# Kernel tuning notes

Hardware: AMD Instinct MI355X
Metric: run time of the kernel (lower is better)

Reference implementation:

```python
import jax, jax.numpy as jnp
import numpy as np
import math

D_MODEL = 1024
N_HEADS = 16
D_K = D_MODEL // N_HEADS
ROPE_BASE = 10000.0


def rope_cos_sin(seq_len, d_k, base=ROPE_BASE, dtype=jnp.float32):
    inv_freq = 1.0 / base ** (jnp.arange(0, d_k, 2, dtype=dtype) / d_k)  # [d_k/2]
    pos = jnp.arange(seq_len, dtype=dtype)
    freqs = jnp.outer(pos, inv_freq)  # [T, d_k/2]
    return jnp.cos(freqs), jnp.sin(freqs)


def apply_rope(x, cos, sin):
    # x: [B, H, T, d_k]; cos/sin: [T, d_k/2]
    x1 = x[..., 0::2]
    x2 = x[..., 1::2]
    c = cos[None, None]
    s = sin[None, None]
    r1 = x1 * c - x2 * s
    r2 = x1 * s + x2 * c
    return jnp.stack([r1, r2], axis=-1).reshape(x.shape)


def setup_inputs() -> dict:
    key = jax.random.key(0)
    ks = jax.random.split(key, 7)
    B, T = 2, 2048
    scale = 1.0 / math.sqrt(D_MODEL)
    return {
        "query": jax.random.normal(ks[0], (B, T, D_MODEL), jnp.float32),
        "key": jax.random.normal(ks[1], (B, T, D_MODEL), jnp.float32),
        "value": jax.random.normal(ks[2], (B, T, D_MODEL), jnp.float32),
        "Wq": jax.random.normal(ks[3], (D_MODEL, D_MODEL), jnp.float32) * scale,
        "Wk": jax.random.normal(ks[4], (D_MODEL, D_MODEL), jnp.float32) * scale,
        "Wv": jax.random.normal(ks[5], (D_MODEL, D_MODEL), jnp.float32) * scale,
        "Wo": jax.random.normal(ks[6], (D_MODEL, D_MODEL), jnp.float32) * scale,
    }


def reference(query, key, value, Wq, Wk, Wv, Wo):
    B, Tq, _ = query.shape
    Tk = key.shape[1]
    # nn.Linear: x @ W.T
    Q = (query @ Wq.T).reshape(B, Tq, N_HEADS, D_K).transpose(0, 2, 1, 3)
    K = (key @ Wk.T).reshape(B, Tk, N_HEADS, D_K).transpose(0, 2, 1, 3)
    V = (value @ Wv.T).reshape(B, Tk, N_HEADS, D_K).transpose(0, 2, 1, 3)
    cos_q, sin_q = rope_cos_sin(Tq, D_K)
    cos_k, sin_k = rope_cos_sin(Tk, D_K)
    Q = apply_rope(Q, cos_q, sin_q)
    K = apply_rope(K, cos_k, sin_k)
    scores = jnp.einsum("bhqd,bhkd->bhqk", Q, K) / math.sqrt(D_K)
    attn = jax.nn.softmax(scores, axis=-1)
    out = jnp.einsum("bhqk,bhkd->bhqd", attn, V)
    out = out.transpose(0, 2, 1, 3).reshape(B, Tq, D_MODEL)
    return out @ Wo.T
```

## Files before the change

kernel.cpp:

```cpp
#include <hip/hip_runtime.h>
#include <hip/hip_bf16.h>
#include <cstdint>

typedef unsigned short u16;
typedef __attribute__((ext_vector_type(4))) float fl4;
typedef __attribute__((ext_vector_type(2))) float fl2;
typedef __attribute__((ext_vector_type(4))) unsigned short u16x4;
typedef __attribute__((ext_vector_type(8))) unsigned short u16x8;
typedef __attribute__((ext_vector_type(2))) unsigned int u32x2;
typedef __attribute__((ext_vector_type(8))) __bf16 bf16x8;
typedef __attribute__((ext_vector_type(4))) float f32x4;

#define MKE 4194304
#define NKE 1048576

static __device__ __forceinline__ u16 f2bf(float x) {
  unsigned int u = __builtin_bit_cast(unsigned int, x);
  u += 0x7fffu + ((u >> 16) & 1u);
  return (u16)(u >> 16);
}

static __device__ __forceinline__ unsigned int cvtpk(float a, float b) {
  unsigned int r;
  asm("v_cvt_pk_bf16_f32 %0, %1, %2" : "=v"(r) : "v"(a), "v"(b));
  return r;
}

static __device__ __forceinline__ f32x4 mfma16(bf16x8 a, bf16x8 b, f32x4 c) {
  return __builtin_amdgcn_mfma_f32_16x16x32_bf16(a, b, c, 0, 0, 0);
}

static __device__ __forceinline__ void gload_lds16(const void* g, void* l) {
  __builtin_amdgcn_global_load_lds((const __attribute__((address_space(1))) void*)g,
                                   (__attribute__((address_space(3))) void*)l,
                                   16, 0, 0);
}

__global__ __launch_bounds__(256) void k_prep(const float* __restrict__ q,
                                              const float* __restrict__ k,
                                              const float* __restrict__ v,
                                              const float* __restrict__ wq,
                                              const float* __restrict__ wk,
                                              const float* __restrict__ wv,
                                              const float* __restrict__ wo,
                                              u16* __restrict__ ws,
                                              float* __restrict__ tab) {
  const int bid = blockIdx.x;
  if (bid >= 16384) {
    const int idx = (bid - 16384) * 256 + threadIdx.x;
    const int t = idx >> 5, i = idx & 31;
    const float ang = (float)t * exp2f(-0.4152410118609203f * (float)i);
    float sn, cs;
    sincosf(ang, &sn, &cs);
    reinterpret_cast<fl2*>(tab)[idx] = (fl2){cs, sn};
    return;
  }
  const int i = bid * 256 + threadIdx.x;
  const float* src;
  u16* dst;
  int loc;
  if (i < 3 * 1048576) {
    const int seg = i >> 20;
    loc = i & 1048575;
    src = seg == 0 ? q : (seg == 1 ? k : v);
    dst = ws + (size_t)seg * MKE;
  } else {
    const int j = i - 3 * 1048576;
    const int seg = j >> 18;
    loc = j & 262143;
    src = seg == 0 ? wq : (seg == 1 ? wk : (seg == 2 ? wv : wo));
    dst = ws + 3 * (size_t)MKE + (size_t)seg * NKE;
  }
  fl4 val = reinterpret_cast<const fl4*>(src)[loc];
  u16x4 o;
  o[0] = f2bf(val[0]); o[1] = f2bf(val[1]); o[2] = f2bf(val[2]); o[3] = f2bf(val[3]);
  reinterpret_cast<u16x4*>(dst)[loc] = o;
}

__global__ __launch_bounds__(256) void k_gemm_qkv(
    const u16* __restrict__ aq, const u16* __restrict__ ak, const u16* __restrict__ av,
    const u16* __restrict__ bq, const u16* __restrict__ bk, const u16* __restrict__ bv,
    u16* __restrict__ cq, u16* __restrict__ ck, u16* __restrict__ cv,
    const fl2* __restrict__ tab) {
  constexpr int K = 1024;
  __shared__ __align__(16) u16 sA[2][128 * 64];
  __shared__ __align__(16) u16 sB[2][64 * 64];
  const int z = blockIdx.z;
  const u16* A  = z == 0 ? aq : (z == 1 ? ak : av);
  const u16* Bw = z == 0 ? bq : (z == 1 ? bk : bv);
  u16* C        = z == 0 ? cq : (z == 1 ? ck : cv);
  const float scale = (z == 0) ? 0.18033688011112042f : 1.0f;

  const int tid = threadIdx.x;
  const int w = tid >> 6, lane = tid & 63;
  const int wm = w >> 1, wn = w & 1;
  const int trow = blockIdx.y << 7, tcol = blockIdx.x << 6;
  const int l15 = lane & 15, l4 = lane >> 4;
  const int srow = lane >> 3;
  const int scol = ((lane & 7) ^ srow) << 3;

  f32x4 acc[4][2];
#pragma unroll
  for (int m = 0; m < 4; ++m)
#pragma unroll
    for (int n = 0; n < 2; ++n) acc[m][n] = (f32x4){0.f, 0.f, 0.f, 0.f};

  auto stage = [&](int k0, int buf) {
#pragma unroll
    for (int c = 0; c < 4; ++c) {
      const int g = c * 4 + w;
      const int row = g * 8 + srow;
      gload_lds16(A + (size_t)(trow + row) * K + (k0 + scol), (void*)(sA[buf] + g * 512));
    }
#pragma unroll
    for (int c = 0; c < 2; ++c) {
      const int g = c * 4 + w;
      const int row = g * 8 + srow;
      gload_lds16(Bw + (size_t)(tcol + row) * K + (k0 + scol), (void*)(sB[buf] + g * 512));
    }
  };

  stage(0, 0);
  __syncthreads();

  for (int t = 0; t < 16; ++t) {
    const int buf = t & 1;
    if (t + 1 < 16) stage((t + 1) * 64, buf ^ 1);
#pragma unroll
    for (int kc = 0; kc < 2; ++kc) {
      const int kb = (kc * 32 + l4 * 8) * 2;
      bf16x8 af[4], bfr[2];
#pragma unroll
      for (int m = 0; m < 4; ++m) {
        const int r = wm * 64 + m * 16 + l15;
        af[m] = *reinterpret_cast<const bf16x8*>(
            reinterpret_cast<const char*>(sA[buf]) + r * 128 + (kb ^ ((r & 7) << 4)));
      }
#pragma unroll
      for (int n = 0; n < 2; ++n) {
        const int r = wn * 32 + n * 16 + l15;
        bfr[n] = *reinterpret_cast<const bf16x8*>(
            reinterpret_cast<const char*>(sB[buf]) + r * 128 + (kb ^ ((r & 7) << 4)));
      }
      __builtin_amdgcn_s_setprio(1);
#pragma unroll
      for (int m = 0; m < 4; ++m)
#pragma unroll
        for (int n = 0; n < 2; ++n)
          acc[m][n] = mfma16(af[m], bfr[n], acc[m][n]);
      __builtin_amdgcn_s_setprio(0);
    }
    __syncthreads();
  }

  const int b = trow >> 11, tb = trow & 2047;
  const int h = tcol >> 6;
  if (z < 2) {
#pragma unroll
    for (int m = 0; m < 4; ++m) {
#pragma unroll
      for (int n = 0; n < 2; ++n) {
#pragma unroll
        for (int r = 0; r < 4; ++r) {
          const float vsc = acc[m][n][r] * scale;
          const int t = tb + wm * 64 + m * 16 + l4 * 4 + r;
          const int d = wn * 32 + n * 16 + l15;
          const float partner = __shfl_xor(vsc, 1);
          const fl2 cs = tab[t * 32 + (d >> 1)];
          const float outv =
              (d & 1) ? (partner * cs.y + vsc * cs.x) : (vsc * cs.x - partner * cs.y);
          C[((size_t)((b << 4) + h) * 2048 + t) * 64 + d] = f2bf(outv);
        }
      }
    }
  } else {
    u16* smem = sA[0];
#pragma unroll
    for (int m = 0; m < 4; ++m)
#pragma unroll
      for (int n = 0; n < 2; ++n)
#pragma unroll
        for (int r = 0; r < 4; ++r) {
          const int dl = wn * 32 + n * 16 + l15;
          const int rl = wm * 64 + m * 16 + l4 * 4 + r;
          smem[dl * 128 + (rl ^ ((dl & 15) * 8))] = f2bf(acc[m][n][r]);
        }
    __syncthreads();
#pragma unroll
    for (int j = 0; j < 4; ++j) {
      const int flat = (tid + j * 256) * 8;
      const int dl = flat >> 7, t0 = flat & 127;
      u16x8 vv = *reinterpret_cast<const u16x8*>(smem + dl * 128 + (t0 ^ ((dl & 15) * 8)));
      u16* dst = C + ((size_t)((b << 4) + h) * 64 + dl) * 2048 + tb + t0;
      *reinterpret_cast<u16x8*>(dst) = vv;
    }
  }
}

__global__ __launch_bounds__(256) void k_gemm_o(const u16* __restrict__ A,
                                                const u16* __restrict__ Bw,
                                                float* __restrict__ C) {
  constexpr int K = 1024, N = 1024;
  __shared__ __align__(16) u16 sA[2][128 * 64];
  __shared__ __align__(16) u16 sB[2][64 * 64];
  const int tid = threadIdx.x;
  const int w = tid >> 6, lane = tid & 63;
  const int wm = w >> 1, wn = w & 1;
  const int trow = blockIdx.y << 7, tcol = blockIdx.x << 6;
  const int l15 = lane & 15, l4 = lane >> 4;
  const int srow = lane >> 3;
  const int scol = ((lane & 7) ^ srow) << 3;

  f32x4 acc[4][2];
#pragma unroll
  for (int m = 0; m < 4; ++m)
#pragma unroll
    for (int n = 0; n < 2; ++n) acc[m][n] = (f32x4){0.f, 0.f, 0.f, 0.f};

  auto stage = [&](int k0, int buf) {
#pragma unroll
    for (int c = 0; c < 4; ++c) {
      const int g = c * 4 + w;
      const int row = g * 8 + srow;
      gload_lds16(A + (size_t)(trow + row) * K + (k0 + scol), (void*)(sA[buf] + g * 512));
    }
#pragma unroll
    for (int c = 0; c < 2; ++c) {
      const int g = c * 4 + w;
      const int row = g * 8 + srow;
      gload_lds16(Bw + (size_t)(tcol + row) * K + (k0 + scol), (void*)(sB[buf] + g * 512));
    }
  };

  stage(0, 0);
  __syncthreads();

  for (int t = 0; t < 16; ++t) {
    const int buf = t & 1;
    if (t + 1 < 16) stage((t + 1) * 64, buf ^ 1);
#pragma unroll
    for (int kc = 0; kc < 2; ++kc) {
      const int kb = (kc * 32 + l4 * 8) * 2;
      bf16x8 af[4], bfr[2];
#pragma unroll
      for (int m = 0; m < 4; ++m) {
        const int r = wm * 64 + m * 16 + l15;
        af[m] = *reinterpret_cast<const bf16x8*>(
            reinterpret_cast<const char*>(sA[buf]) + r * 128 + (kb ^ ((r & 7) << 4)));
      }
#pragma unroll
      for (int n = 0; n < 2; ++n) {
        const int r = wn * 32 + n * 16 + l15;
        bfr[n] = *reinterpret_cast<const bf16x8*>(
            reinterpret_cast<const char*>(sB[buf]) + r * 128 + (kb ^ ((r & 7) << 4)));
      }
      __builtin_amdgcn_s_setprio(1);
#pragma unroll
      for (int m = 0; m < 4; ++m)
#pragma unroll
        for (int n = 0; n < 2; ++n)
          acc[m][n] = mfma16(af[m], bfr[n], acc[m][n]);
      __builtin_amdgcn_s_setprio(0);
    }
    __syncthreads();
  }

#pragma unroll
  for (int m = 0; m < 4; ++m)
#pragma unroll
    for (int n = 0; n < 2; ++n)
#pragma unroll
      for (int r = 0; r < 4; ++r) {
        const int row = trow + wm * 64 + m * 16 + l4 * 4 + r;
        const int col = tcol + wn * 32 + n * 16 + l15;
        C[(size_t)row * N + col] = acc[m][n][r];
      }
}

__global__ __launch_bounds__(256) void k_attn(const u16* __restrict__ Q,
                                              const u16* __restrict__ Kh,
                                              const u16* __restrict__ Vt,
                                              u16* __restrict__ Oout) {
  __shared__ __align__(16) char lds[81920];
  const int tid = threadIdx.x;
  const int w = tid >> 6, lane = tid & 63;
  const int l15 = lane & 15, l4 = lane >> 4;
  const int nb = blockIdx.x;
  const int xcd = nb & 7, idx = nb >> 3;
  const int bh = xcd * 4 + (idx >> 4);
  const int q0 = (idx & 15) << 7;

  const u16* Qg = Q + (size_t)bh * (2048 * 64);
  const u16* Kg = Kh + (size_t)bh * (2048 * 64);
  const u16* Vg = Vt + (size_t)bh * (64 * 2048);

  const int swz = (l15 & 7) << 4;
  const int rk0 = l15 * 128 + ((l4 * 16) ^ swz);
  const int rk1 = rk0 ^ 64;
  const int pbase = 65536 + w * 4096 + l15 * 128;
  int pwvA[4];
#pragma unroll
  for (int nn = 0; nn < 4; ++nn) pwvA[nn] = pbase + (((nn * 32) | (l4 * 8)) ^ swz);
  const int rpA0 = pbase + ((l4 * 16) ^ swz);
  const int rpA1 = rpA0 ^ 64;
  const int wst = w * 1024;

  const int srow8 = lane >> 3;
  const int scol = ((lane & 7) ^ srow8) << 3;
  const u16* gK = Kg + (size_t)(w * 8 + srow8) * 64 + scol;
  const u16* gV = Vg + (size_t)(w * 8 + srow8) * 2048 + scol;

  bf16x8 qf0, qf1, qf2, qf3;
  {
    const u16* qpA = Qg + (size_t)(q0 + w * 32 + l15) * 64 + l4 * 8;
    qf0 = *reinterpret_cast<const bf16x8*>(qpA);
    qf1 = *reinterpret_cast<const bf16x8*>(qpA + 32);
    const u16* qpB = qpA + 16 * 64;
    qf2 = *reinterpret_cast<const bf16x8*>(qpB);
    qf3 = *reinterpret_cast<const bf16x8*>(qpB + 32);
  }

  f32x4 oA[4], oB[4];
#pragma unroll
  for (int nn = 0; nn < 4; ++nn) {
    oA[nn] = (f32x4){0.f, 0.f, 0.f, 0.f};
    oB[nn] = (f32x4){0.f, 0.f, 0.f, 0.f};
  }
  float lrunA = 0.f, lrunB = 0.f;

#define STAGE_CUR(BUF)                                                           \
  {                                                                              \
    gload_lds16(gK,        lds + (BUF) + wst);                                   \
    gload_lds16(gK + 2048, lds + (BUF) + wst + 4096);                            \
    gload_lds16(gK + 4096, lds + (BUF) + wst + 8192);                            \
    gload_lds16(gK + 6144, lds + (BUF) + wst + 12288);                           \
    gload_lds16(gV,               lds + 32768 + (BUF) + wst);                    \
    gload_lds16(gV + 65536,       lds + 32768 + (BUF) + wst + 4096);             \
    gload_lds16(gV + 64,          lds + 32768 + (BUF) + wst + 8192);             \
    gload_lds16(gV + 65536 + 64,  lds + 32768 + (BUF) + wst + 12288);            \
    gK += 8192; gV += 128;                                                       \
  }

#define QKT(KOFF, SA, SB)                                                        \
  {                                                                              \
    __builtin_amdgcn_s_setprio(1);                                               \
    _Pragma("unroll")                                                            \
    for (int nn = 0; nn < 4; ++nn) {                                             \
      bf16x8 kf = *(const bf16x8*)(lds + (KOFF) + rk0 + nn * 2048);              \
      SA[nn] = mfma16(kf, qf0, (f32x4){0.f, 0.f, 0.f, 0.f});                     \
      SB[nn] = mfma16(kf, qf2, (f32x4){0.f, 0.f, 0.f, 0.f});                     \
    }                                                                            \
    _Pragma("unroll")                                                            \
    for (int nn = 0; nn < 4; ++nn) {                                             \
      bf16x8 kf = *(const bf16x8*)(lds + (KOFF) + rk1 + nn * 2048);              \
      SA[nn] = mfma16(kf, qf1, SA[nn]);                                          \
      SB[nn] = mfma16(kf, qf3, SB[nn]);                                          \
    }                                                                            \
    __builtin_amdgcn_s_setprio(0);                                               \
  }

#define SOFTMAX(SA, SB, PKA, PKB, RSA, RSB)                                      \
  {                                                                              \
    float ppA[4][4], ppB[4][4];                                                  \
    _Pragma("unroll")                                                            \
    for (int nn = 0; nn < 4; ++nn) {                                             \
      ppA[nn][0] = __builtin_amdgcn_exp2f(SA[nn][0]);                            \
      ppA[nn][1] = __builtin_amdgcn_exp2f(SA[nn][1]);                            \
      ppA[nn][2] = __builtin_amdgcn_exp2f(SA[nn][2]);                            \
      ppA[nn][3] = __builtin_amdgcn_exp2f(SA[nn][3]);                            \
      ppB[nn][0] = __builtin_amdgcn_exp2f(SB[nn][0]);                            \
      ppB[nn][1] = __builtin_amdgcn_exp2f(SB[nn][1]);                            \
      ppB[nn][2] = __builtin_amdgcn_exp2f(SB[nn][2]);                            \
      ppB[nn][3] = __builtin_amdgcn_exp2f(SB[nn][3]);                            \
    }                                                                            \
    _Pragma("unroll")                                                            \
    for (int nn = 0; nn < 4; ++nn) {                                             \
      PKA[nn][0] = cvtpk(ppA[nn][0], ppA[nn][1]);                                \
      PKA[nn][1] = cvtpk(ppA[nn][2], ppA[nn][3]);                                \
      PKB[nn][0] = cvtpk(ppB[nn][0], ppB[nn][1]);                                \
      PKB[nn][1] = cvtpk(ppB[nn][2], ppB[nn][3]);                                \
    }                                                                            \
    RSA = ((ppA[0][0] + ppA[0][1]) + (ppA[0][2] + ppA[0][3])) +                  \
          ((ppA[1][0] + ppA[1][1]) + (ppA[1][2] + ppA[1][3])) +                  \
          ((ppA[2][0] + ppA[2][1]) + (ppA[2][2] + ppA[2][3])) +                  \
          ((ppA[3][0] + ppA[3][1]) + (ppA[3][2] + ppA[3][3]));                   \
    RSB = ((ppB[0][0] + ppB[0][1]) + (ppB[0][2] + ppB[0][3])) +                  \
          ((ppB[1][0] + ppB[1][1]) + (ppB[1][2] + ppB[1][3])) +                  \
          ((ppB[2][0] + ppB[2][1]) + (ppB[2][2] + ppB[2][3])) +                  \
          ((ppB[3][0] + ppB[3][1]) + (ppB[3][2] + ppB[3][3]));                   \
  }

#define PWRITE(PKA, PKB)                                                         \
  {                                                                              \
    _Pragma("unroll")                                                            \
    for (int nn = 0; nn < 4; ++nn) {                                             \
      *(u32x2*)(lds + pwvA[nn]) = PKA[nn];                                       \
      *(u32x2*)(lds + pwvA[nn] + 2048) = PKB[nn];                                \
    }                                                                            \
  }

#define PV(VOFF)                                                                 \
  {                                                                              \
    __builtin_amdgcn_s_setprio(1);                                               \
    _Pragma("unroll")                                                            \
    for (int kc = 0; kc < 2; ++kc) {                                             \
      const bf16x8 pfA = *(const bf16x8*)(lds + (kc ? rpA1 : rpA0));             \
      const bf16x8 pfB = *(const bf16x8*)(lds + (kc ? rpA1 : rpA0) + 2048);      \
      const int rkk = kc ? rk1 : rk0;                                            \
      _Pragma("unroll")                                                          \
      for (int nn = 0; nn < 4; ++nn) {                                           \
        bf16x8 vf = *(const bf16x8*)(lds + (VOFF) + rkk + nn * 2048);            \
        oA[nn] = mfma16(pfA, vf, oA[nn]);                                        \
        oB[nn] = mfma16(pfB, vf, oB[nn]);                                        \
      }                                                                          \
    }                                                                            \
    __builtin_amdgcn_s_setprio(0);                                               \
  }

  STAGE_CUR(0)
  __syncthreads();

  int cur = 0;
  for (int c = 0; c < 16; ++c) {
    if (c < 15) STAGE_CUR(cur ^ 16384)
    f32x4 s0A[4], s0B[4], s1A[4], s1B[4];
    QKT(cur, s0A, s0B)
    QKT(cur + 8192, s1A, s1B)
    u32x2 pk0A[4], pk0B[4], pk1A[4], pk1B[4];
    float rs0A, rs0B, rs1A, rs1B;
    SOFTMAX(s0A, s0B, pk0A, pk0B, rs0A, rs0B)
    PWRITE(pk0A, pk0B)
    SOFTMAX(s1A, s1B, pk1A, pk1B, rs1A, rs1B)
    rs0A += __shfl_xor(rs0A, 16); rs0A += __shfl_xor(rs0A, 32);
    rs0B += __shfl_xor(rs0B, 16); rs0B += __shfl_xor(rs0B, 32);
    lrunA += rs0A; lrunB += rs0B;
    PV(32768 + cur)
    PWRITE(pk1A, pk1B)
    rs1A += __shfl_xor(rs1A, 16); rs1A += __shfl_xor(rs1A, 32);
    rs1B += __shfl_xor(rs1B, 16); rs1B += __shfl_xor(rs1B, 32);
    lrunA += rs1A; lrunB += rs1B;
    PV(32768 + cur + 8192)
    __syncthreads();
    cur ^= 16384;
  }
#undef PV
#undef PWRITE
#undef SOFTMAX
#undef QKT
#undef STAGE_CUR

  const int b = bh >> 4, h = bh & 15;
  float lrA[4], lrB[4];
#pragma unroll
  for (int r = 0; r < 4; ++r) {
    const int src = (lane & 48) | (l4 * 4 + r);
    lrA[r] = 1.f / __shfl(lrunA, src);
    lrB[r] = 1.f / __shfl(lrunB, src);
  }
#pragma unroll
  for (int nn = 0; nn < 4; ++nn)
#pragma unroll
    for (int r = 0; r < 4; ++r) {
      const int tA = q0 + w * 32 + l4 * 4 + r;
      const int d = nn * 16 + l15;
      Oout[((size_t)(b * 2048 + tA)) * 1024 + h * 64 + d] = f2bf(oA[nn][r] * lrA[r]);
      Oout[((size_t)(b * 2048 + tA + 16)) * 1024 + h * 64 + d] = f2bf(oB[nn][r] * lrB[r]);
    }
}

extern "C" void kernel_launch(void* const* d_in, const int* in_sizes, int n_in,
                              void* d_out, int out_size, void* d_ws, size_t ws_size,
                              hipStream_t stream) {
  const float* q  = (const float*)d_in[0];
  const float* k  = (const float*)d_in[1];
  const float* v  = (const float*)d_in[2];
  const float* wq = (const float*)d_in[3];
  const float* wk = (const float*)d_in[4];
  const float* wv = (const float*)d_in[5];
  const float* wo = (const float*)d_in[6];

  u16* ws = (u16*)d_ws;
  u16* Xq  = ws;
  u16* Xk  = Xq + MKE;
  u16* Xv  = Xk + MKE;
  u16* Wqb = Xv + MKE;
  u16* Wkb = Wqb + NKE;
  u16* Wvb = Wkb + NKE;
  u16* Wob = Wvb + NKE;
  u16* Qr  = Wob + NKE;
  u16* Kr  = Qr + MKE;
  u16* Vtm = Kr + MKE;
  u16* Vtr = Vtm + MKE;
  u16* AO  = Vtr + MKE;
  float* tab = (float*)AO;

  k_prep<<<16640, 256, 0, stream>>>(q, k, v, wq, wk, wv, wo, ws, tab);
  k_gemm_qkv<<<dim3(16, 32, 3), 256, 0, stream>>>(Xq, Xk, Xv, Wqb, Wkb, Wvb,
                                                  Qr, Kr, Vtr, (const fl2*)tab);
  k_attn<<<512, 256, 0, stream>>>(Qr, Kr, Vtr, AO);
  k_gemm_o<<<dim3(16, 32), 256, 0, stream>>>(AO, Wob, (float*)d_out);
}
```

Baseline: 126.4 us.

## Split attention work across 8 waves with 16 query rows each

```diff
diff --git a/kernel.cpp b/kernel.cpp
--- a/kernel.cpp
+++ b/kernel.cpp
@@ -277,10 +277,10 @@
       }
 }
 
-__global__ __launch_bounds__(256) void k_attn(const u16* __restrict__ Q,
-                                              const u16* __restrict__ Kh,
-                                              const u16* __restrict__ Vt,
-                                              u16* __restrict__ Oout) {
+__global__ __launch_bounds__(512, 4) void k_attn(const u16* __restrict__ Q,
+                                                 const u16* __restrict__ Kh,
+                                                 const u16* __restrict__ Vt,
+                                                 u16* __restrict__ Oout) {
   __shared__ __align__(16) char lds[81920];
   const int tid = threadIdx.x;
   const int w = tid >> 6, lane = tid & 63;
@@ -297,12 +297,12 @@
   const int swz = (l15 & 7) << 4;
   const int rk0 = l15 * 128 + ((l4 * 16) ^ swz);
   const int rk1 = rk0 ^ 64;
-  const int pbase = 65536 + w * 4096 + l15 * 128;
-  int pwvA[4];
-#pragma unroll
-  for (int nn = 0; nn < 4; ++nn) pwvA[nn] = pbase + (((nn * 32) | (l4 * 8)) ^ swz);
-  const int rpA0 = pbase + ((l4 * 16) ^ swz);
-  const int rpA1 = rpA0 ^ 64;
+  const int pbase = 65536 + w * 2048 + l15 * 128;
+  int pwv[4];
+#pragma unroll
+  for (int nn = 0; nn < 4; ++nn) pwv[nn] = pbase + (((nn * 32) | (l4 * 8)) ^ swz);
+  const int rp0 = pbase + ((l4 * 16) ^ swz);
+  const int rp1 = rp0 ^ 64;
   const int wst = w * 1024;
 
   const int srow8 = lane >> 3;
@@ -310,93 +310,68 @@
   const u16* gK = Kg + (size_t)(w * 8 + srow8) * 64 + scol;
   const u16* gV = Vg + (size_t)(w * 8 + srow8) * 2048 + scol;
 
-  bf16x8 qf0, qf1, qf2, qf3;
+  bf16x8 qf0, qf1;
   {
-    const u16* qpA = Qg + (size_t)(q0 + w * 32 + l15) * 64 + l4 * 8;
-    qf0 = *reinterpret_cast<const bf16x8*>(qpA);
-    qf1 = *reinterpret_cast<const bf16x8*>(qpA + 32);
-    const u16* qpB = qpA + 16 * 64;
-    qf2 = *reinterpret_cast<const bf16x8*>(qpB);
-    qf3 = *reinterpret_cast<const bf16x8*>(qpB + 32);
-  }
-
-  f32x4 oA[4], oB[4];
-#pragma unroll
-  for (int nn = 0; nn < 4; ++nn) {
-    oA[nn] = (f32x4){0.f, 0.f, 0.f, 0.f};
-    oB[nn] = (f32x4){0.f, 0.f, 0.f, 0.f};
-  }
-  float lrunA = 0.f, lrunB = 0.f;
+    const u16* qp = Qg + (size_t)(q0 + w * 16 + l15) * 64 + l4 * 8;
+    qf0 = *reinterpret_cast<const bf16x8*>(qp);
+    qf1 = *reinterpret_cast<const bf16x8*>(qp + 32);
+  }
+
+  f32x4 o[4];
+#pragma unroll
+  for (int nn = 0; nn < 4; ++nn) o[nn] = (f32x4){0.f, 0.f, 0.f, 0.f};
+  float lrun = 0.f;
 
 #define STAGE_CUR(BUF)                                                           \
   {                                                                              \
-    gload_lds16(gK,        lds + (BUF) + wst);                                   \
-    gload_lds16(gK + 2048, lds + (BUF) + wst + 4096);                            \
-    gload_lds16(gK + 4096, lds + (BUF) + wst + 8192);                            \
-    gload_lds16(gK + 6144, lds + (BUF) + wst + 12288);                           \
-    gload_lds16(gV,               lds + 32768 + (BUF) + wst);                    \
-    gload_lds16(gV + 65536,       lds + 32768 + (BUF) + wst + 4096);             \
-    gload_lds16(gV + 64,          lds + 32768 + (BUF) + wst + 8192);             \
-    gload_lds16(gV + 65536 + 64,  lds + 32768 + (BUF) + wst + 12288);            \
+    gload_lds16(gK,        lds + (BUF) + wst);                 \
+    gload_lds16(gK + 4096, lds + (BUF) + 8192 + wst);          \
+    gload_lds16(gV,        lds + 32768 + (BUF) + wst);         \
+    gload_lds16(gV + 64,   lds + 32768 + (BUF) + 8192 + wst);  \
     gK += 8192; gV += 128;                                                       \
   }
 
-#define QKT(KOFF, SA, SB)                                                        \
+#define QKT(KOFF, S)                                                             \
   {                                                                              \
     __builtin_amdgcn_s_setprio(1);                                               \
     _Pragma("unroll")                                                            \
     for (int nn = 0; nn < 4; ++nn) {                                             \
       bf16x8 kf = *(const bf16x8*)(lds + (KOFF) + rk0 + nn * 2048);              \
-      SA[nn] = mfma16(kf, qf0, (f32x4){0.f, 0.f, 0.f, 0.f});                     \
-      SB[nn] = mfma16(kf, qf2, (f32x4){0.f, 0.f, 0.f, 0.f});                     \
+      S[nn] = mfma16(kf, qf0, (f32x4){0.f, 0.f, 0.f, 0.f});                      \
     }                                                                            \
     _Pragma("unroll")                                                            \
     for (int nn = 0; nn < 4; ++nn) {                                             \
       bf16x8 kf = *(const bf16x8*)(lds + (KOFF) + rk1 + nn * 2048);              \
-      SA[nn] = mfma16(kf, qf1, SA[nn]);                                          \
-      SB[nn] = mfma16(kf, qf3, SB[nn]);                                          \
+      S[nn] = mfma16(kf, qf1, S[nn]);                                            \
     }                                                                            \
     __builtin_amdgcn_s_setprio(0);                                               \
   }
 
-#define SOFTMAX(SA, SB, PKA, PKB, RSA, RSB)                                      \
+#define SOFTMAX(S, PK, RS)                                                       \
   {                                                                              \
-    float ppA[4][4], ppB[4][4];                                                  \
+    float pp[4][4];                                                              \
     _Pragma("unroll")                                                            \
     for (int nn = 0; nn < 4; ++nn) {                                             \
-      ppA[nn][0] = __builtin_amdgcn_exp2f(SA[nn][0]);                            \
-      ppA[nn][1] = __builtin_amdgcn_exp2f(SA[nn][1]);                            \
-      ppA[nn][2] = __builtin_amdgcn_exp2f(SA[nn][2]);                            \
-      ppA[nn][3] = __builtin_amdgcn_exp2f(SA[nn][3]);                            \
-      ppB[nn][0] = __builtin_amdgcn_exp2f(SB[nn][0]);                            \
-      ppB[nn][1] = __builtin_amdgcn_exp2f(SB[nn][1]);                            \
-      ppB[nn][2] = __builtin_amdgcn_exp2f(SB[nn][2]);                            \
-      ppB[nn][3] = __builtin_amdgcn_exp2f(SB[nn][3]);                            \
+      pp[nn][0] = __builtin_amdgcn_exp2f(S[nn][0]);                              \
+      pp[nn][1] = __builtin_amdgcn_exp2f(S[nn][1]);                              \
+      pp[nn][2] = __builtin_amdgcn_exp2f(S[nn][2]);                              \
+      pp[nn][3] = __builtin_amdgcn_exp2f(S[nn][3]);                              \
     }                                                                            \
     _Pragma("unroll")                                                            \
     for (int nn = 0; nn < 4; ++nn) {                                             \
-      PKA[nn][0] = cvtpk(ppA[nn][0], ppA[nn][1]);                                \
-      PKA[nn][1] = cvtpk(ppA[nn][2], ppA[nn][3]);                                \
-      PKB[nn][0] = cvtpk(ppB[nn][0], ppB[nn][1]);                                \
-      PKB[nn][1] = cvtpk(ppB[nn][2], ppB[nn][3]);                                \
+      PK[nn][0] = cvtpk(pp[nn][0], pp[nn][1]);                                   \
+      PK[nn][1] = cvtpk(pp[nn][2], pp[nn][3]);                                   \
     }                                                                            \
-    RSA = ((ppA[0][0] + ppA[0][1]) + (ppA[0][2] + ppA[0][3])) +                  \
-          ((ppA[1][0] + ppA[1][1]) + (ppA[1][2] + ppA[1][3])) +                  \
-          ((ppA[2][0] + ppA[2][1]) + (ppA[2][2] + ppA[2][3])) +                  \
-          ((ppA[3][0] + ppA[3][1]) + (ppA[3][2] + ppA[3][3]));                   \
-    RSB = ((ppB[0][0] + ppB[0][1]) + (ppB[0][2] + ppB[0][3])) +                  \
-          ((ppB[1][0] + ppB[1][1]) + (ppB[1][2] + ppB[1][3])) +                  \
-          ((ppB[2][0] + ppB[2][1]) + (ppB[2][2] + ppB[2][3])) +                  \
-          ((ppB[3][0] + ppB[3][1]) + (ppB[3][2] + ppB[3][3]));                   \
-  }
-
-#define PWRITE(PKA, PKB)                                                         \
+    RS = ((pp[0][0] + pp[0][1]) + (pp[0][2] + pp[0][3])) +                       \
+         ((pp[1][0] + pp[1][1]) + (pp[1][2] + pp[1][3])) +                       \
+         ((pp[2][0] + pp[2][1]) + (pp[2][2] + pp[2][3])) +                       \
+         ((pp[3][0] + pp[3][1]) + (pp[3][2] + pp[3][3]));                        \
+  }
+
+#define PWRITE(PK)                                                               \
   {                                                                              \
     _Pragma("unroll")                                                            \
-    for (int nn = 0; nn < 4; ++nn) {                                             \
-      *(u32x2*)(lds + pwvA[nn]) = PKA[nn];                                       \
-      *(u32x2*)(lds + pwvA[nn] + 2048) = PKB[nn];                                \
-    }                                                                            \
+    for (int nn = 0; nn < 4; ++nn) *(u32x2*)(lds + pwv[nn]) = PK[nn];            \
   }
 
 #define PV(VOFF)                                                                 \
@@ -404,14 +379,12 @@
     __builtin_amdgcn_s_setprio(1);                                               \
     _Pragma("unroll")                                                            \
     for (int kc = 0; kc < 2; ++kc) {                                             \
-      const bf16x8 pfA = *(const bf16x8*)(lds + (kc ? rpA1 : rpA0));             \
-      const bf16x8 pfB = *(const bf16x8*)(lds + (kc ? rpA1 : rpA0) + 2048);      \
+      const bf16x8 pf = *(const bf16x8*)(lds + (kc ? rp1 : rp0));                \
       const int rkk = kc ? rk1 : rk0;                                            \
       _Pragma("unroll")                                                          \
       for (int nn = 0; nn < 4; ++nn) {                                           \
         bf16x8 vf = *(const bf16x8*)(lds + (VOFF) + rkk + nn * 2048);            \
-        oA[nn] = mfma16(pfA, vf, oA[nn]);                                        \
-        oB[nn] = mfma16(pfB, vf, oB[nn]);                                        \
+        o[nn] = mfma16(pf, vf, o[nn]);                                           \
       }                                                                          \
     }                                                                            \
     __builtin_amdgcn_s_setprio(0);                                               \
@@ -423,22 +396,20 @@
   int cur = 0;
   for (int c = 0; c < 16; ++c) {
     if (c < 15) STAGE_CUR(cur ^ 16384)
-    f32x4 s0A[4], s0B[4], s1A[4], s1B[4];
-    QKT(cur, s0A, s0B)
-    QKT(cur + 8192, s1A, s1B)
-    u32x2 pk0A[4], pk0B[4], pk1A[4], pk1B[4];
-    float rs0A, rs0B, rs1A, rs1B;
-    SOFTMAX(s0A, s0B, pk0A, pk0B, rs0A, rs0B)
-    PWRITE(pk0A, pk0B)
-    SOFTMAX(s1A, s1B, pk1A, pk1B, rs1A, rs1B)
-    rs0A += __shfl_xor(rs0A, 16); rs0A += __shfl_xor(rs0A, 32);
-    rs0B += __shfl_xor(rs0B, 16); rs0B += __shfl_xor(rs0B, 32);
-    lrunA += rs0A; lrunB += rs0B;
+    f32x4 s0[4], s1[4];
+    QKT(cur, s0)
+    QKT(cur + 8192, s1)
+    u32x2 pk0[4], pk1[4];
+    float rs0, rs1;
+    SOFTMAX(s0, pk0, rs0)
+    PWRITE(pk0)
+    SOFTMAX(s1, pk1, rs1)
+    rs0 += __shfl_xor(rs0, 16); rs0 += __shfl_xor(rs0, 32);
+    lrun += rs0;
     PV(32768 + cur)
-    PWRITE(pk1A, pk1B)
-    rs1A += __shfl_xor(rs1A, 16); rs1A += __shfl_xor(rs1A, 32);
-    rs1B += __shfl_xor(rs1B, 16); rs1B += __shfl_xor(rs1B, 32);
-    lrunA += rs1A; lrunB += rs1B;
+    PWRITE(pk1)
+    rs1 += __shfl_xor(rs1, 16); rs1 += __shfl_xor(rs1, 32);
+    lrun += rs1;
     PV(32768 + cur + 8192)
     __syncthreads();
     cur ^= 16384;
@@ -450,21 +421,17 @@
 #undef STAGE_CUR
 
   const int b = bh >> 4, h = bh & 15;
-  float lrA[4], lrB[4];
-#pragma unroll
-  for (int r = 0; r < 4; ++r) {
-    const int src = (lane & 48) | (l4 * 4 + r);
-    lrA[r] = 1.f / __shfl(lrunA, src);
-    lrB[r] = 1.f / __shfl(lrunB, src);
-  }
+  float lr[4];
+#pragma unroll
+  for (int r = 0; r < 4; ++r)
+    lr[r] = 1.f / __shfl(lrun, (lane & 48) | (l4 * 4 + r));
 #pragma unroll
   for (int nn = 0; nn < 4; ++nn)
 #pragma unroll
     for (int r = 0; r < 4; ++r) {
-      const int tA = q0 + w * 32 + l4 * 4 + r;
+      const int t = q0 + w * 16 + l4 * 4 + r;
       const int d = nn * 16 + l15;
-      Oout[((size_t)(b * 2048 + tA)) * 1024 + h * 64 + d] = f2bf(oA[nn][r] * lrA[r]);
-      Oout[((size_t)(b * 2048 + tA + 16)) * 1024 + h * 64 + d] = f2bf(oB[nn][r] * lrB[r]);
+      Oout[((size_t)(b * 2048 + t)) * 1024 + h * 64 + d] = f2bf(o[nn][r] * lr[r]);
     }
 }
 
@@ -497,6 +464,6 @@
   k_prep<<<16640, 256, 0, stream>>>(q, k, v, wq, wk, wv, wo, ws, tab);
   k_gemm_qkv<<<dim3(16, 32, 3), 256, 0, stream>>>(Xq, Xk, Xv, Wqb, Wkb, Wvb,
                                                   Qr, Kr, Vtr, (const fl2*)tab);
-  k_attn<<<512, 256, 0, stream>>>(Qr, Kr, Vtr, AO);
+  k_attn<<<512, 512, 0, stream>>>(Qr, Kr, Vtr, AO);
   k_gemm_o<<<dim3(16, 32), 256, 0, stream>>>(AO, Wob, (float*)d_out);
 }
```

Measured after the change: 123.5 us. -2.3%, faster.
